# Kernel optimization log

Measured on AMD Instinct MI355X. Metric: run time of the kernel, lower is better.

## Reference

```python
import jax, jax.numpy as jnp
import numpy as np

B, S, IN, OUT = 4, 32, 8192, 8192


def setup_inputs() -> dict:
    key = jax.random.key(0)
    k1, k2, k3, k4 = jax.random.split(key, 4)
    x = jax.random.normal(k1, (B, S, IN), dtype=jnp.float32)
    # FP8-e4m3 stored weight: round-trip through fp8 so values are representable,
    # then keep as fp32 (the module upcasts to fp32 before the matmul anyway).
    w = jax.random.normal(k2, (OUT, IN), dtype=jnp.float32)
    weight = w.astype(jnp.float8_e4m3fn).astype(jnp.float32)
    # per-output-channel scale, strictly positive small values
    weight_scale = jax.random.uniform(k3, (OUT, 1), dtype=jnp.float32,
                                      minval=1e-3, maxval=2e-2)
    bias = (jax.random.normal(k4, (OUT,), dtype=jnp.float32) * 0.01).astype(jnp.float16)
    return {"x": x, "weight": weight, "weight_scale": weight_scale, "bias": bias}


def reference(x, weight, weight_scale, bias):
    # dequantize fp8 weight to fp32 with per-channel scale  [OUT, IN]
    dq_w = weight * weight_scale
    # x @ dq_w.T  -> [B, S, OUT]
    out = jnp.einsum("bsi,oi->bso", x.astype(jnp.float32), dq_w)
    out = out + bias.astype(jnp.float32)
    return out
```

## Files before the change

### kernel.cpp

```cpp
#include <hip/hip_runtime.h>
#include <hip/hip_bf16.h>
#include <hip/hip_fp16.h>


namespace {
constexpr int MM = 128;
constexpr int NN = 8192;
constexpr int KK = 8192;
constexpr int KSPLIT = 8;
constexpr int KPB = KK / KSPLIT;
constexpr int KT = 128;
constexpr int NIT = KPB / KT;
constexpr int LDSW = KT + 8;

constexpr size_t WS_SCALE_OFF = 0;
constexpr size_t WS_BIAS_OFF  = 8192 * 4;
constexpr size_t WS_XSW_OFF   = 65536;
constexpr size_t WS_NEED      = WS_XSW_OFF + (size_t)MM * KK * 2;

typedef __attribute__((ext_vector_type(8))) short bf16x8;
typedef __attribute__((ext_vector_type(4))) float f32x4;
}

__global__ __launch_bounds__(256)
void cfp8_prep(const float* __restrict__ x,
               const float* __restrict__ c1, const float* __restrict__ c2,
               unsigned char* __restrict__ ws)
{
    const int bid = blockIdx.x;
    const int tid = threadIdx.x;

    if (bid < 32) {
        __shared__ int s_c1s, s_kind;
        if (tid < 64) {
            float v = c1[tid * 64];
            unsigned long long b = __ballot((v > 1e-4f) && (v < 0.5f));
            int c1s = (b == ~0ull) ? 1 : 0;
            const void* bp = c1s ? (const void*)c2 : (const void*)c1;
            float vf = __half2float(((const __half*)bp)[tid * 64]);
            unsigned long long bf_ = __ballot((vf < 0.5f) && (vf > -0.5f));
            float vb = __bfloat162float(((const __hip_bfloat16*)bp)[tid * 64]);
            unsigned long long bb = __ballot((vb < 0.5f) && (vb > -0.5f));
            if (tid == 0) {
                s_c1s  = c1s;
                s_kind = (bf_ == ~0ull) ? 0 : ((bb == ~0ull) ? 1 : 2);
            }
        }
        __syncthreads();
        const float* scalep = s_c1s ? c1 : c2;
        const void*  biasp  = s_c1s ? (const void*)c2 : (const void*)c1;
        const int i = bid * 256 + tid;
        float bsv;
        if (s_kind == 0)      bsv = __half2float(((const __half*)biasp)[i]);
        else if (s_kind == 1) bsv = __bfloat162float(((const __hip_bfloat16*)biasp)[i]);
        else                  bsv = ((const float*)biasp)[i];
        ((float*)(ws + WS_SCALE_OFF))[i] = scalep[i];
        ((float*)(ws + WS_BIAS_OFF))[i]  = bsv;
    } else {
        const int g = (bid - 32) * 256 + tid;
        const float4* src = (const float4*)x + (size_t)g * 2;
        float4 a = src[0], b = src[1];
        const int m  = g >> 10;
        const int kg = g & 1023;
        const int s  = kg >> 2;
        const int r8 = kg & 3;
        const int t  = m >> 4;
        const int lm = m & 15;
        const int l  = r8 * 16 + lm;
        union { __hip_bfloat16 h[8]; uint4 u; } p;
        p.h[0] = __float2bfloat16(a.x); p.h[1] = __float2bfloat16(a.y);
        p.h[2] = __float2bfloat16(a.z); p.h[3] = __float2bfloat16(a.w);
        p.h[4] = __float2bfloat16(b.x); p.h[5] = __float2bfloat16(b.y);
        p.h[6] = __float2bfloat16(b.z); p.h[7] = __float2bfloat16(b.w);
        ((uint4*)(ws + WS_XSW_OFF))[(size_t)(s * 8 + t) * 64 + l] = p.u;
    }
}

__global__ __launch_bounds__(256, 4)
void cfp8_gemm(const float* __restrict__ w, const unsigned char* __restrict__ ws,
               float* __restrict__ out)
{
    __shared__ __align__(16) __hip_bfloat16 lw[4][2][16 * LDSW];

    const int tid  = threadIdx.x;
    const int lane = tid & 63;
    const int wid  = tid >> 6;
    const int kz   = blockIdx.y;
    const int n0   = blockIdx.x * 64 + wid * 16;
    const size_t kbase = (size_t)kz * KPB;

    const __hip_bfloat16* xsw = (const __hip_bfloat16*)(ws + WS_XSW_OFF);
    const float* wsc = (const float*)(ws + WS_SCALE_OFF);
    const float* wbs = (const float*)(ws + WS_BIAS_OFF);

    const int l16  = lane & 15;
    const int quad = lane >> 4;

    const float sc = wsc[n0 + l16];
    const float bs = (kz == 0) ? wbs[n0 + l16] : 0.0f;

    const int srow = lane >> 5;
    const int scol = (lane & 31) * 4;
    const float* wg = w + (size_t)(n0 + srow) * KK + kbase + scol;

    float4 wf[8];
#pragma unroll
    for (int i = 0; i < 8; ++i)
        wf[i] = *(const float4*)(wg + (size_t)(2 * i) * KK);

    f32x4 acc[8];
#pragma unroll
    for (int t = 0; t < 8; ++t) acc[t] = (f32x4){0.f, 0.f, 0.f, 0.f};

    for (int kt = 0; kt < NIT; ++kt) {
        __hip_bfloat16* lb = &lw[wid][kt & 1][0];

#pragma unroll
        for (int i = 0; i < 8; ++i) {
            union { __hip_bfloat16 h[4]; uint2 u; } p;
            p.h[0] = __float2bfloat16(wf[i].x);
            p.h[1] = __float2bfloat16(wf[i].y);
            p.h[2] = __float2bfloat16(wf[i].z);
            p.h[3] = __float2bfloat16(wf[i].w);
            *(uint2*)&lb[(2 * i + srow) * LDSW + scol] = p.u;
        }

        if (kt + 1 < NIT) {
            const float* wgn = wg + (size_t)(kt + 1) * KT;
#pragma unroll
            for (int i = 0; i < 8; ++i)
                wf[i] = *(const float4*)(wgn + (size_t)(2 * i) * KK);
        }

        const int sgl0 = kz * 32 + kt * 4;
#pragma unroll
        for (int ss = 0; ss < 4; ++ss) {
            bf16x8 bfrag = *(const bf16x8*)&lb[l16 * LDSW + ss * 32 + quad * 8];
            const uint4* xp = (const uint4*)xsw + (size_t)(sgl0 + ss) * 8 * 64 + lane;
            bf16x8 af[8];
#pragma unroll
            for (int t = 0; t < 8; ++t) {
                uint4 u = xp[(size_t)t * 64];
                af[t] = *(bf16x8*)&u;
            }
#pragma unroll
            for (int t = 0; t < 8; ++t)
                acc[t] = __builtin_amdgcn_mfma_f32_16x16x32_bf16(
                    af[t], bfrag, acc[t], 0, 0, 0);
        }
    }

#pragma unroll
    for (int t = 0; t < 8; ++t) {
#pragma unroll
        for (int r = 0; r < 4; ++r) {
            atomicAdd(out + (size_t)(t * 16 + quad * 4 + r) * NN + n0 + l16,
                      acc[t][r] * sc + bs);
        }
    }
}

namespace fb {
constexpr int NT = 64;
constexpr int KTf = 32;
constexpr int NITf = KPB / KTf;
constexpr int LDSP = KTf + 8;
}

__global__ __launch_bounds__(256, 4)
void cfp8lin_mfma2(const float* __restrict__ x, const float* __restrict__ w,
                   const float* __restrict__ c1, const float* __restrict__ c2,
                   float* __restrict__ out)
{
    using namespace fb;
    __shared__ __align__(16) __hip_bfloat16 lx[2][MM * LDSP];
    __shared__ __align__(16) __hip_bfloat16 lw[2][NT * LDSP];
    __shared__ float s_scale[NT];
    __shared__ float s_bias[NT];
    __shared__ int s_c1_is_scale;
    __shared__ int s_bias_kind;

    const int tid = threadIdx.x;
    const int n0 = blockIdx.x * NT;
    const int kz = blockIdx.y;
    const size_t kbase = (size_t)kz * KPB;

    if (tid < 64) {
        float v = c1[tid * 64];
        unsigned long long b = __ballot((v > 1e-4f) && (v < 0.5f));
        int c1s = (b == ~0ull) ? 1 : 0;
        const void* bp = c1s ? (const void*)c2 : (const void*)c1;
        float vf = __half2float(((const __half*)bp)[tid * 64]);
        unsigned long long bf_ = __ballot((vf < 0.5f) && (vf > -0.5f));
        float vb = __bfloat162float(((const __hip_bfloat16*)bp)[tid * 64]);
        unsigned long long bb = __ballot((vb < 0.5f) && (vb > -0.5f));
        if (tid == 0) {
            s_c1_is_scale = c1s;
            s_bias_kind = (bf_ == ~0ull) ? 0 : ((bb == ~0ull) ? 1 : 2);
        }
    }

    const int lrow = tid >> 3;
    const int lc4  = tid & 7;
    const float* xg = x + (size_t)lrow * KK + kbase + lc4 * 4;
    const float* wg = w + (size_t)(n0 + lrow) * KK + kbase + lc4 * 4;

    float4 xv[4], wv[2];
    auto load_tile = [&](int kt) {
        const size_t ko = (size_t)kt * KTf;
#pragma unroll
        for (int i = 0; i < 4; ++i)
            xv[i] = *(const float4*)(xg + (size_t)(i * 32) * KK + ko);
#pragma unroll
        for (int i = 0; i < 2; ++i)
            wv[i] = *(const float4*)(wg + (size_t)(i * 32) * KK + ko);
    };
    load_tile(0);

    const int lane = tid & 63;
    const int wid  = tid >> 6;
    const int wm0  = wid * 32;
    const int l16  = lane & 15;
    const int quad = lane >> 4;
    const int kcol = quad * 8;

    f32x4 acc[2][4];
#pragma unroll
    for (int i = 0; i < 2; ++i)
#pragma unroll
        for (int j = 0; j < 4; ++j) acc[i][j] = (f32x4){0.f, 0.f, 0.f, 0.f};

    for (int kt = 0; kt < NITf; ++kt) {
        const int buf = kt & 1;
#pragma unroll
        for (int i = 0; i < 4; ++i) {
            union { __hip_bfloat16 b[4]; uint2 u; } p;
            p.b[0] = __float2bfloat16(xv[i].x); p.b[1] = __float2bfloat16(xv[i].y);
            p.b[2] = __float2bfloat16(xv[i].z); p.b[3] = __float2bfloat16(xv[i].w);
            *(uint2*)&lx[buf][(i * 32 + lrow) * LDSP + lc4 * 4] = p.u;
        }
#pragma unroll
        for (int i = 0; i < 2; ++i) {
            union { __hip_bfloat16 b[4]; uint2 u; } p;
            p.b[0] = __float2bfloat16(wv[i].x); p.b[1] = __float2bfloat16(wv[i].y);
            p.b[2] = __float2bfloat16(wv[i].z); p.b[3] = __float2bfloat16(wv[i].w);
            *(uint2*)&lw[buf][(i * 32 + lrow) * LDSP + lc4 * 4] = p.u;
        }
        load_tile((kt + 1 < NITf) ? (kt + 1) : 0);
        __syncthreads();
        bf16x8 af[2], bw[4];
#pragma unroll
        for (int i = 0; i < 2; ++i)
            af[i] = *(const bf16x8*)&lx[buf][(wm0 + i * 16 + l16) * LDSP + kcol];
#pragma unroll
        for (int j = 0; j < 4; ++j)
            bw[j] = *(const bf16x8*)&lw[buf][(j * 16 + l16) * LDSP + kcol];
#pragma unroll
        for (int i = 0; i < 2; ++i)
#pragma unroll
            for (int j = 0; j < 4; ++j)
                acc[i][j] = __builtin_amdgcn_mfma_f32_16x16x32_bf16(
                    af[i], bw[j], acc[i][j], 0, 0, 0);
    }

    __syncthreads();
    const float* scalep = s_c1_is_scale ? c1 : c2;
    const void*  biasp  = s_c1_is_scale ? (const void*)c2 : (const void*)c1;
    if (tid < fb::NT) {
        s_scale[tid] = scalep[n0 + tid];
        float b = 0.0f;
        if (kz == 0) {
            if (s_bias_kind == 0)      b = __half2float(((const __half*)biasp)[n0 + tid]);
            else if (s_bias_kind == 1) b = __bfloat162float(((const __hip_bfloat16*)biasp)[n0 + tid]);
            else                       b = ((const float*)biasp)[n0 + tid];
        }
        s_bias[tid] = b;
    }
    __syncthreads();

#pragma unroll
    for (int j = 0; j < 4; ++j) {
        const int nl = j * 16 + l16;
        const float scv = s_scale[nl];
        const float bsv = s_bias[nl];
#pragma unroll
        for (int i = 0; i < 2; ++i) {
            const int mb = wm0 + i * 16 + quad * 4;
#pragma unroll
            for (int r = 0; r < 4; ++r)
                atomicAdd(out + (size_t)(mb + r) * NN + n0 + nl,
                          acc[i][j][r] * scv + bsv);
        }
    }
}

extern "C" void kernel_launch(void* const* d_in, const int* in_sizes, int n_in,
                              void* d_out, int out_size, void* d_ws, size_t ws_size,
                              hipStream_t stream) {
    int iw = 0;
    for (int i = 1; i < n_in; ++i) if (in_sizes[i] > in_sizes[iw]) iw = i;
    int ix = -1;
    for (int i = 0; i < n_in; ++i)
        if (i != iw && (ix < 0 || in_sizes[i] > in_sizes[ix])) ix = i;
    const float* c1 = nullptr;
    const float* c2 = nullptr;
    for (int i = 0; i < n_in; ++i) {
        if (i == iw || i == ix) continue;
        if (!c1) c1 = (const float*)d_in[i];
        else     c2 = (const float*)d_in[i];
    }
    const float* w = (const float*)d_in[iw];
    const float* x = (const float*)d_in[ix];
    float* out = (float*)d_out;

    hipMemsetAsync(d_out, 0, (size_t)out_size * sizeof(float), stream);

    if (ws_size >= WS_NEED && d_ws != nullptr) {
        unsigned char* ws = (unsigned char*)d_ws;
        cfp8_prep<<<dim3(32 + 512), dim3(256), 0, stream>>>(x, c1, c2, ws);
        cfp8_gemm<<<dim3(NN / 64, KSPLIT), dim3(256), 0, stream>>>(w, ws, out);
    } else {
        dim3 grid(NN / fb::NT, KSPLIT);
        cfp8lin_mfma2<<<grid, dim3(256), 0, stream>>>(x, w, c1, c2, out);
    }
}
```

Baseline: 417.9 us.

## Fuse x bf16 conversion into GEMM and stream weights directly to registers

Removes the separate prep kernel and workspace: each GEMM block loads its fp32 x slice, converts it to bf16, and double-buffers it in LDS. Weight fragments are loaded straight from global into registers for the MFMA B operand, so the weight LDS staging is gone. The K-split is halved to 4 and occupancy is lowered to 2 blocks per CU, which reduces atomic traffic but leaves fewer blocks to fill the GPU.

```diff
diff --git a/kernel.cpp b/kernel.cpp
--- a/kernel.cpp
+++ b/kernel.cpp
@@ -7,182 +7,41 @@
 constexpr int MM = 128;
 constexpr int NN = 8192;
 constexpr int KK = 8192;
-constexpr int KSPLIT = 8;
+constexpr int KSPLIT = 4;
 constexpr int KPB = KK / KSPLIT;
 constexpr int KT = 128;
-constexpr int NIT = KPB / KT;
-constexpr int LDSW = KT + 8;
-
-constexpr size_t WS_SCALE_OFF = 0;
-constexpr size_t WS_BIAS_OFF  = 8192 * 4;
-constexpr size_t WS_XSW_OFF   = 65536;
-constexpr size_t WS_NEED      = WS_XSW_OFF + (size_t)MM * KK * 2;
+constexpr int NCH = KPB / KT;
+constexpr int NKS = KPB / 32;
+constexpr int LDSX = KT + 8;
 
 typedef __attribute__((ext_vector_type(8))) short bf16x8;
 typedef __attribute__((ext_vector_type(4))) float f32x4;
+
+__device__ __forceinline__ bf16x8 pack8(float4 a, float4 b) {
+    union { __hip_bfloat16 h[8]; bf16x8 v; } p;
+    p.h[0] = __float2bfloat16(a.x); p.h[1] = __float2bfloat16(a.y);
+    p.h[2] = __float2bfloat16(a.z); p.h[3] = __float2bfloat16(a.w);
+    p.h[4] = __float2bfloat16(b.x); p.h[5] = __float2bfloat16(b.y);
+    p.h[6] = __float2bfloat16(b.z); p.h[7] = __float2bfloat16(b.w);
+    return p.v;
+}
 }
 
-__global__ __launch_bounds__(256)
-void cfp8_prep(const float* __restrict__ x,
-               const float* __restrict__ c1, const float* __restrict__ c2,
-               unsigned char* __restrict__ ws)
+__global__ __launch_bounds__(256, 2)
+void cfp8_gemm_nws(const float* __restrict__ x, const float* __restrict__ w,
+                   const float* __restrict__ c1, const float* __restrict__ c2,
+                   float* __restrict__ out)
 {
-    const int bid = blockIdx.x;
-    const int tid = threadIdx.x;
-
-    if (bid < 32) {
-        __shared__ int s_c1s, s_kind;
-        if (tid < 64) {
-            float v = c1[tid * 64];
-            unsigned long long b = __ballot((v > 1e-4f) && (v < 0.5f));
-            int c1s = (b == ~0ull) ? 1 : 0;
-            const void* bp = c1s ? (const void*)c2 : (const void*)c1;
-            float vf = __half2float(((const __half*)bp)[tid * 64]);
-            unsigned long long bf_ = __ballot((vf < 0.5f) && (vf > -0.5f));
-            float vb = __bfloat162float(((const __hip_bfloat16*)bp)[tid * 64]);
-            unsigned long long bb = __ballot((vb < 0.5f) && (vb > -0.5f));
-            if (tid == 0) {
-                s_c1s  = c1s;
-                s_kind = (bf_ == ~0ull) ? 0 : ((bb == ~0ull) ? 1 : 2);
-            }
-        }
-        __syncthreads();
-        const float* scalep = s_c1s ? c1 : c2;
-        const void*  biasp  = s_c1s ? (const void*)c2 : (const void*)c1;
-        const int i = bid * 256 + tid;
-        float bsv;
-        if (s_kind == 0)      bsv = __half2float(((const __half*)biasp)[i]);
-        else if (s_kind == 1) bsv = __bfloat162float(((const __hip_bfloat16*)biasp)[i]);
-        else                  bsv = ((const float*)biasp)[i];
-        ((float*)(ws + WS_SCALE_OFF))[i] = scalep[i];
-        ((float*)(ws + WS_BIAS_OFF))[i]  = bsv;
-    } else {
-        const int g = (bid - 32) * 256 + tid;
-        const float4* src = (const float4*)x + (size_t)g * 2;
-        float4 a = src[0], b = src[1];
-        const int m  = g >> 10;
-        const int kg = g & 1023;
-        const int s  = kg >> 2;
-        const int r8 = kg & 3;
-        const int t  = m >> 4;
-        const int lm = m & 15;
-        const int l  = r8 * 16 + lm;
-        union { __hip_bfloat16 h[8]; uint4 u; } p;
-        p.h[0] = __float2bfloat16(a.x); p.h[1] = __float2bfloat16(a.y);
-        p.h[2] = __float2bfloat16(a.z); p.h[3] = __float2bfloat16(a.w);
-        p.h[4] = __float2bfloat16(b.x); p.h[5] = __float2bfloat16(b.y);
-        p.h[6] = __float2bfloat16(b.z); p.h[7] = __float2bfloat16(b.w);
-        ((uint4*)(ws + WS_XSW_OFF))[(size_t)(s * 8 + t) * 64 + l] = p.u;
-    }
-}
-
-__global__ __launch_bounds__(256, 4)
-void cfp8_gemm(const float* __restrict__ w, const unsigned char* __restrict__ ws,
-               float* __restrict__ out)
-{
-    __shared__ __align__(16) __hip_bfloat16 lw[4][2][16 * LDSW];
+    __shared__ __align__(16) __hip_bfloat16 lx[2][MM * LDSX];
+    __shared__ int s_c1s, s_kind;
 
     const int tid  = threadIdx.x;
     const int lane = tid & 63;
     const int wid  = tid >> 6;
+    const int l16  = lane & 15;
+    const int quad = lane >> 4;
     const int kz   = blockIdx.y;
     const int n0   = blockIdx.x * 64 + wid * 16;
-    const size_t kbase = (size_t)kz * KPB;
-
-    const __hip_bfloat16* xsw = (const __hip_bfloat16*)(ws + WS_XSW_OFF);
-    const float* wsc = (const float*)(ws + WS_SCALE_OFF);
-    const float* wbs = (const float*)(ws + WS_BIAS_OFF);
-
-    const int l16  = lane & 15;
-    const int quad = lane >> 4;
-
-    const float sc = wsc[n0 + l16];
-    const float bs = (kz == 0) ? wbs[n0 + l16] : 0.0f;
-
-    const int srow = lane >> 5;
-    const int scol = (lane & 31) * 4;
-    const float* wg = w + (size_t)(n0 + srow) * KK + kbase + scol;
-
-    float4 wf[8];
-#pragma unroll
-    for (int i = 0; i < 8; ++i)
-        wf[i] = *(const float4*)(wg + (size_t)(2 * i) * KK);
-
-    f32x4 acc[8];
-#pragma unroll
-    for (int t = 0; t < 8; ++t) acc[t] = (f32x4){0.f, 0.f, 0.f, 0.f};
-
-    for (int kt = 0; kt < NIT; ++kt) {
-        __hip_bfloat16* lb = &lw[wid][kt & 1][0];
-
-#pragma unroll
-        for (int i = 0; i < 8; ++i) {
-            union { __hip_bfloat16 h[4]; uint2 u; } p;
-            p.h[0] = __float2bfloat16(wf[i].x);
-            p.h[1] = __float2bfloat16(wf[i].y);
-            p.h[2] = __float2bfloat16(wf[i].z);
-            p.h[3] = __float2bfloat16(wf[i].w);
-            *(uint2*)&lb[(2 * i + srow) * LDSW + scol] = p.u;
-        }
-
-        if (kt + 1 < NIT) {
-            const float* wgn = wg + (size_t)(kt + 1) * KT;
-#pragma unroll
-            for (int i = 0; i < 8; ++i)
-                wf[i] = *(const float4*)(wgn + (size_t)(2 * i) * KK);
-        }
-
-        const int sgl0 = kz * 32 + kt * 4;
-#pragma unroll
-        for (int ss = 0; ss < 4; ++ss) {
-            bf16x8 bfrag = *(const bf16x8*)&lb[l16 * LDSW + ss * 32 + quad * 8];
-            const uint4* xp = (const uint4*)xsw + (size_t)(sgl0 + ss) * 8 * 64 + lane;
-            bf16x8 af[8];
-#pragma unroll
-            for (int t = 0; t < 8; ++t) {
-                uint4 u = xp[(size_t)t * 64];
-                af[t] = *(bf16x8*)&u;
-            }
-#pragma unroll
-            for (int t = 0; t < 8; ++t)
-                acc[t] = __builtin_amdgcn_mfma_f32_16x16x32_bf16(
-                    af[t], bfrag, acc[t], 0, 0, 0);
-        }
-    }
-
-#pragma unroll
-    for (int t = 0; t < 8; ++t) {
-#pragma unroll
-        for (int r = 0; r < 4; ++r) {
-            atomicAdd(out + (size_t)(t * 16 + quad * 4 + r) * NN + n0 + l16,
-                      acc[t][r] * sc + bs);
-        }
-    }
-}
-
-namespace fb {
-constexpr int NT = 64;
-constexpr int KTf = 32;
-constexpr int NITf = KPB / KTf;
-constexpr int LDSP = KTf + 8;
-}
-
-__global__ __launch_bounds__(256, 4)
-void cfp8lin_mfma2(const float* __restrict__ x, const float* __restrict__ w,
-                   const float* __restrict__ c1, const float* __restrict__ c2,
-                   float* __restrict__ out)
-{
-    using namespace fb;
-    __shared__ __align__(16) __hip_bfloat16 lx[2][MM * LDSP];
-    __shared__ __align__(16) __hip_bfloat16 lw[2][NT * LDSP];
-    __shared__ float s_scale[NT];
-    __shared__ float s_bias[NT];
-    __shared__ int s_c1_is_scale;
-    __shared__ int s_bias_kind;
-
-    const int tid = threadIdx.x;
-    const int n0 = blockIdx.x * NT;
-    const int kz = blockIdx.y;
     const size_t kbase = (size_t)kz * KPB;
 
     if (tid < 64) {
@@ -195,101 +54,90 @@
         float vb = __bfloat162float(((const __hip_bfloat16*)bp)[tid * 64]);
         unsigned long long bb = __ballot((vb < 0.5f) && (vb > -0.5f));
         if (tid == 0) {
-            s_c1_is_scale = c1s;
-            s_bias_kind = (bf_ == ~0ull) ? 0 : ((bb == ~0ull) ? 1 : 2);
+            s_c1s  = c1s;
+            s_kind = (bf_ == ~0ull) ? 0 : ((bb == ~0ull) ? 1 : 2);
+        }
+    }
+    __syncthreads();
+    const float* scalep = s_c1s ? c1 : c2;
+    const void*  biasp  = s_c1s ? (const void*)c2 : (const void*)c1;
+    const float sc = scalep[n0 + l16];
+    float bs = 0.0f;
+    if (kz == 0) {
+        if (s_kind == 0)      bs = __half2float(((const __half*)biasp)[n0 + l16]);
+        else if (s_kind == 1) bs = __bfloat162float(((const __hip_bfloat16*)biasp)[n0 + l16]);
+        else                  bs = ((const float*)biasp)[n0 + l16];
+    }
+
+    const int srow = tid >> 1;
+    const int shf  = tid & 1;
+    const float* xrow = x + (size_t)srow * KK + kbase + shf * 64;
+
+    const float* wlane = w + (size_t)(n0 + l16) * KK + kbase + quad * 8;
+
+    float4 sr[16];
+#pragma unroll
+    for (int i = 0; i < 16; ++i) sr[i] = *(const float4*)(xrow + i * 4);
+
+    float4 wa = *(const float4*)(wlane);
+    float4 wb = *(const float4*)(wlane + 4);
+
+#pragma unroll
+    for (int j = 0; j < 8; ++j) {
+        bf16x8 v = pack8(sr[2 * j], sr[2 * j + 1]);
+        *(bf16x8*)&lx[0][srow * LDSX + shf * 64 + j * 8] = v;
+    }
+    __syncthreads();
+
+    f32x4 acc[8];
+#pragma unroll
+    for (int t = 0; t < 8; ++t) acc[t] = (f32x4){0.f, 0.f, 0.f, 0.f};
+
+    for (int c = 0; c < NCH; ++c) {
+        const int buf = c & 1;
+
+        if (c + 1 < NCH) {
+#pragma unroll
+            for (int i = 0; i < 16; ++i)
+                sr[i] = *(const float4*)(xrow + (c + 1) * KT + i * 4);
+        }
+        __builtin_amdgcn_sched_barrier(0);
+
+#pragma unroll
+        for (int s = 0; s < 4; ++s) {
+            const int ksn = (c * 4 + s + 1 < NKS) ? (c * 4 + s + 1) : (NKS - 1);
+            const float* wn = wlane + (size_t)ksn * 32;
+            float4 na = *(const float4*)(wn);
+            float4 nb = *(const float4*)(wn + 4);
+
+            bf16x8 bfrag = pack8(wa, wb);
+            bf16x8 af[8];
+#pragma unroll
+            for (int t = 0; t < 8; ++t)
+                af[t] = *(const bf16x8*)&lx[buf][(t * 16 + l16) * LDSX + s * 32 + quad * 8];
+#pragma unroll
+            for (int t = 0; t < 8; ++t)
+                acc[t] = __builtin_amdgcn_mfma_f32_16x16x32_bf16(af[t], bfrag, acc[t], 0, 0, 0);
+
+            wa = na; wb = nb;
+        }
+
+        if (c + 1 < NCH) {
+#pragma unroll
+            for (int j = 0; j < 8; ++j) {
+                bf16x8 v = pack8(sr[2 * j], sr[2 * j + 1]);
+                *(bf16x8*)&lx[buf ^ 1][srow * LDSX + shf * 64 + j * 8] = v;
+            }
+            __syncthreads();
         }
     }
 
-    const int lrow = tid >> 3;
-    const int lc4  = tid & 7;
-    const float* xg = x + (size_t)lrow * KK + kbase + lc4 * 4;
-    const float* wg = w + (size_t)(n0 + lrow) * KK + kbase + lc4 * 4;
-
-    float4 xv[4], wv[2];
-    auto load_tile = [&](int kt) {
-        const size_t ko = (size_t)kt * KTf;
 #pragma unroll
-        for (int i = 0; i < 4; ++i)
-            xv[i] = *(const float4*)(xg + (size_t)(i * 32) * KK + ko);
+    for (int t = 0; t < 8; ++t) {
 #pragma unroll
-        for (int i = 0; i < 2; ++i)
-            wv[i] = *(const float4*)(wg + (size_t)(i * 32) * KK + ko);
-    };
-    load_tile(0);
-
-    const int lane = tid & 63;
-    const int wid  = tid >> 6;
-    const int wm0  = wid * 32;
-    const int l16  = lane & 15;
-    const int quad = lane >> 4;
-    const int kcol = quad * 8;
-
-    f32x4 acc[2][4];
-#pragma unroll
-    for (int i = 0; i < 2; ++i)
-#pragma unroll
-        for (int j = 0; j < 4; ++j) acc[i][j] = (f32x4){0.f, 0.f, 0.f, 0.f};
-
-    for (int kt = 0; kt < NITf; ++kt) {
-        const int buf = kt & 1;
-#pragma unroll
-        for (int i = 0; i < 4; ++i) {
-            union { __hip_bfloat16 b[4]; uint2 u; } p;
-            p.b[0] = __float2bfloat16(xv[i].x); p.b[1] = __float2bfloat16(xv[i].y);
-            p.b[2] = __float2bfloat16(xv[i].z); p.b[3] = __float2bfloat16(xv[i].w);
-            *(uint2*)&lx[buf][(i * 32 + lrow) * LDSP + lc4 * 4] = p.u;
-        }
-#pragma unroll
-        for (int i = 0; i < 2; ++i) {
-            union { __hip_bfloat16 b[4]; uint2 u; } p;
-            p.b[0] = __float2bfloat16(wv[i].x); p.b[1] = __float2bfloat16(wv[i].y);
-            p.b[2] = __float2bfloat16(wv[i].z); p.b[3] = __float2bfloat16(wv[i].w);
-            *(uint2*)&lw[buf][(i * 32 + lrow) * LDSP + lc4 * 4] = p.u;
-        }
-        load_tile((kt + 1 < NITf) ? (kt + 1) : 0);
-        __syncthreads();
-        bf16x8 af[2], bw[4];
-#pragma unroll
-        for (int i = 0; i < 2; ++i)
-            af[i] = *(const bf16x8*)&lx[buf][(wm0 + i * 16 + l16) * LDSP + kcol];
-#pragma unroll
-        for (int j = 0; j < 4; ++j)
-            bw[j] = *(const bf16x8*)&lw[buf][(j * 16 + l16) * LDSP + kcol];
-#pragma unroll
-        for (int i = 0; i < 2; ++i)
-#pragma unroll
-            for (int j = 0; j < 4; ++j)
-                acc[i][j] = __builtin_amdgcn_mfma_f32_16x16x32_bf16(
-                    af[i], bw[j], acc[i][j], 0, 0, 0);
-    }
-
-    __syncthreads();
-    const float* scalep = s_c1_is_scale ? c1 : c2;
-    const void*  biasp  = s_c1_is_scale ? (const void*)c2 : (const void*)c1;
-    if (tid < fb::NT) {
-        s_scale[tid] = scalep[n0 + tid];
-        float b = 0.0f;
-        if (kz == 0) {
-            if (s_bias_kind == 0)      b = __half2float(((const __half*)biasp)[n0 + tid]);
-            else if (s_bias_kind == 1) b = __bfloat162float(((const __hip_bfloat16*)biasp)[n0 + tid]);
-            else                       b = ((const float*)biasp)[n0 + tid];
-        }
-        s_bias[tid] = b;
-    }
-    __syncthreads();
-
-#pragma unroll
-    for (int j = 0; j < 4; ++j) {
-        const int nl = j * 16 + l16;
-        const float scv = s_scale[nl];
-        const float bsv = s_bias[nl];
-#pragma unroll
-        for (int i = 0; i < 2; ++i) {
-            const int mb = wm0 + i * 16 + quad * 4;
-#pragma unroll
-            for (int r = 0; r < 4; ++r)
-                atomicAdd(out + (size_t)(mb + r) * NN + n0 + nl,
-                          acc[i][j][r] * scv + bsv);
+        for (int r = 0; r < 4; ++r) {
+            atomicAdd(out + (size_t)(t * 16 + quad * 4 + r) * NN + n0 + l16,
+                      acc[t][r] * sc + bs);
         }
     }
 }
@@ -313,14 +161,8 @@
     const float* x = (const float*)d_in[ix];
     float* out = (float*)d_out;
 
+    (void)d_ws; (void)ws_size;
+
     hipMemsetAsync(d_out, 0, (size_t)out_size * sizeof(float), stream);
-
-    if (ws_size >= WS_NEED && d_ws != nullptr) {
-        unsigned char* ws = (unsigned char*)d_ws;
-        cfp8_prep<<<dim3(32 + 512), dim3(256), 0, stream>>>(x, c1, c2, ws);
-        cfp8_gemm<<<dim3(NN / 64, KSPLIT), dim3(256), 0, stream>>>(w, ws, out);
-    } else {
-        dim3 grid(NN / fb::NT, KSPLIT);
-        cfp8lin_mfma2<<<grid, dim3(256), 0, stream>>>(x, w, c1, c2, out);
-    }
+    cfp8_gemm_nws<<<dim3(NN / 64, KSPLIT), dim3(256), 0, stream>>>(x, w, c1, c2, out);
 }
```

Result: slower. 432.7 us (+3.6%).
